# Optimization experiments

Measured on AMD Instinct MI355X. Metric: run time of the kernel, lower is better.

The kernel has to match this reference:

```python
import jax, jax.numpy as jnp
import numpy as np

SIZE = 8
STRIDES = (4, 8, 16)
QSCALE = 0.25
QMIN, QMAX = -32768, 32767  # qint16


def fake_quant(x):
    # QuantStub with FixedScaleObserver scale=0.25, qint16
    return jnp.clip(jnp.round(x / QSCALE), QMIN, QMAX) * QSCALE


def roi_align(f, rois, size):
    """torchvision.ops.RoIAlign(output_size=size, spatial_scale=1, sampling_ratio=1, aligned=False).
    f: [N,C,H,W], rois: [A,5] = (batch_idx, x1, y1, x2, y2) -> [A,C,size,size]."""
    N, C, H, W = f.shape
    b = rois[:, 0].astype(jnp.int32)
    x1, y1, x2, y2 = rois[:, 1], rois[:, 2], rois[:, 3], rois[:, 4]
    roi_w = jnp.maximum(x2 - x1, 1.0)
    roi_h = jnp.maximum(y2 - y1, 1.0)
    centers = jnp.arange(size, dtype=f.dtype) + 0.5  # sampling_ratio=1 -> bin center
    y = y1[:, None] + centers[None, :] * (roi_h / size)[:, None]  # [A,S]
    x = x1[:, None] + centers[None, :] * (roi_w / size)[:, None]  # [A,S]

    def prep(c, L):
        valid = (c >= -1.0) & (c <= L)
        c = jnp.maximum(c, 0.0)
        low0 = jnp.floor(c).astype(jnp.int32)
        hi_edge = low0 >= L - 1
        low = jnp.where(hi_edge, L - 1, low0)
        high = jnp.where(hi_edge, L - 1, low0 + 1)
        c = jnp.where(hi_edge, jnp.asarray(L - 1, c.dtype), c)
        frac = c - low.astype(c.dtype)
        return low, high, frac, valid

    yl, yh, fy, vy = prep(y, H)
    xl, xh, fx, vx = prep(x, W)

    ff = f.transpose(0, 2, 3, 1).reshape(N * H * W, C)  # channels-last flat for gather

    def gather(yy, xx):
        idx = (b[:, None, None] * H + yy[:, :, None]) * W + xx[:, None, :]  # [A,S,S]
        return ff[idx]  # [A,S,S,C]

    wy0 = (1.0 - fy)[:, :, None, None]
    wy1 = fy[:, :, None, None]
    wx0 = (1.0 - fx)[:, None, :, None]
    wx1 = fx[:, None, :, None]
    val = (gather(yl, xl) * wy0 * wx0 + gather(yl, xh) * wy0 * wx1
           + gather(yh, xl) * wy1 * wx0 + gather(yh, xh) * wy1 * wx1)
    mask = (vy[:, :, None] & vx[:, None, :])[..., None]
    val = jnp.where(mask, val, 0.0)
    return val.transpose(0, 3, 1, 2)  # [A,C,S,S]


def generate_rois(pixel, batch_index, size):
    bi = batch_index.astype(pixel.dtype)[:, None]
    rois = []
    for s in STRIDES:
        tl = jnp.maximum(pixel / s - size / 2.0, 0.0)
        br = jnp.maximum(pixel / s + size / 2.0, 0.0)
        rois.append(fake_quant(jnp.concatenate([bi, tl, br], axis=-1)))
    return rois


def setup_inputs() -> dict:
    key = jax.random.key(0)
    k0, k1, k2, kp, kb = jax.random.split(key, 5)
    f0 = jax.random.normal(k0, (4, 64, 256, 256), jnp.float32)
    f1 = jax.random.normal(k1, (4, 64, 128, 128), jnp.float32)
    f2 = jax.random.normal(k2, (4, 64, 64, 64), jnp.float32)
    pixel = jax.random.uniform(kp, (4096, 2), jnp.float32) * 1008.0  # raster-map coords
    batch_index = jax.random.randint(kb, (4096,), 0, 4, jnp.int32)
    return {"f0": f0, "f1": f1, "f2": f2, "pixel": pixel, "batch_index": batch_index}


def reference(f0, f1, f2, pixel, batch_index):
    rois = generate_rois(pixel, batch_index, SIZE)
    feats = [roi_align(f, r, SIZE) for f, r in zip((f0, f1, f2), rois)]
    return jnp.concatenate(feats, axis=1)  # [A, sum(C_i), SIZE, SIZE]
```

## Files before the change

### kernel.cpp

```cpp
#include <hip/hip_runtime.h>


#define NCH 64

typedef unsigned int  u32;
typedef unsigned short u16;

__device__ __forceinline__ float fake_quant(float v) {
    float r = rintf(v * 4.0f);
    r = fminf(fmaxf(r, -32768.0f), 32767.0f);
    return r * 0.25f;
}

struct Prep { int lo, hi; float fr; bool valid; };
__device__ __forceinline__ Prep prep(float c, int L) {
    Prep r;
    r.valid = (c >= -1.0f) && (c <= (float)L);
    c = fmaxf(c, 0.0f);
    const int l0 = (int)floorf(c);
    const bool he = (l0 >= L - 1);
    r.lo = he ? (L - 1) : l0;
    r.hi = he ? (L - 1) : (l0 + 1);
    r.fr = (he ? (float)(L - 1) : c) - (float)r.lo;
    return r;
}

__device__ __forceinline__ u16 f2bf(float x) {
    u32 u = __float_as_uint(x);
    u += 0x7FFFu + ((u >> 16) & 1u);
    return (u16)(u >> 16);
}
__device__ __forceinline__ float bflo(u32 w) { return __uint_as_float(w << 16); }
__device__ __forceinline__ float bfhi(u32 w) { return __uint_as_float(w & 0xFFFF0000u); }

__global__ __launch_bounds__(256) void nchw_to_nhwc_bf16(
    const float* __restrict__ f0, const float* __restrict__ f1,
    const float* __restrict__ f2, u16* __restrict__ n0,
    u16* __restrict__ n1, u16* __restrict__ n2)
{
    __shared__ float tile[64][65];
    const int t = threadIdx.x;
    const int b = blockIdx.y;
    const int g = blockIdx.x;
    const float* src; u16* dst; int HW; int tl;
    if (g < 1024)      { src = f0; dst = n0; HW = 65536; tl = g; }
    else if (g < 1280) { src = f1; dst = n1; HW = 16384; tl = g - 1024; }
    else               { src = f2; dst = n2; HW = 4096;  tl = g - 1280; }
    const int hw0 = tl * 64;
    const float* __restrict__ s = src + (size_t)b * 64 * HW + hw0;
    u32* __restrict__ d = (u32*)(dst + ((size_t)b * HW + hw0) * 64);

    const int x  = t & 63;
    const int ph = t >> 6;
    #pragma unroll
    for (int k = 0; k < 16; ++k) {
        const int c = ph * 16 + k;
        tile[c][x] = __builtin_nontemporal_load(s + (size_t)c * HW + x);
    }
    __syncthreads();
    #pragma unroll
    for (int k = 0; k < 8; ++k) {
        const int idx = k * 256 + t;
        const int pos = idx >> 5;
        const int cp  = idx & 31;
        const u32 w = (u32)f2bf(tile[2 * cp][pos])
                    | ((u32)f2bf(tile[2 * cp + 1][pos]) << 16);
        __builtin_nontemporal_store(w, d + pos * 32 + cp);
    }
}

__global__ __launch_bounds__(256) void cropper_qat_bf16(
    const u16* __restrict__ g0, const u16* __restrict__ g1,
    const u16* __restrict__ g2, const float* __restrict__ pixel,
    const int* __restrict__ bidx, float* __restrict__ out)
{
    __shared__ uint4 tile[81 * 8];

    const int a   = blockIdx.x;
    const int lvl = blockIdx.y;

    const float inv_s = (lvl == 0) ? 0.25f : (lvl == 1) ? 0.125f : 0.0625f;
    const int   L     = (lvl == 0) ? 256   : (lvl == 1) ? 128    : 64;
    const u16* __restrict__ f = (lvl == 0) ? g0 : (lvl == 1) ? g1 : g2;

    const int   b  = bidx[a];
    const float px = pixel[2 * a];
    const float py = pixel[2 * a + 1];

    const float x1 = fake_quant(fmaxf(px * inv_s - 4.0f, 0.0f));
    const float y1 = fake_quant(fmaxf(py * inv_s - 4.0f, 0.0f));
    const float x2 = fake_quant(fmaxf(px * inv_s + 4.0f, 0.0f));
    const float y2 = fake_quant(fmaxf(py * inv_s + 4.0f, 0.0f));

    const float binw = fmaxf(x2 - x1, 1.0f) * 0.125f;
    const float binh = fmaxf(y2 - y1, 1.0f) * 0.125f;

    const int y_lo = prep(y1 + 0.5f * binh, L).lo;
    const int x_lo = prep(x1 + 0.5f * binw, L).lo;

    const int tid = threadIdx.x;

    {
        const u16* __restrict__ fbase =
            f + ((size_t)b * L * L + (size_t)y_lo * L + x_lo) * NCH;
        #pragma unroll
        for (int it = 0; it < 3; ++it) {
            const int g = tid + it * 256;
            if (g < 648) {
                const int ly  = g / 72;
                const int rem = g - ly * 72;
                const int pos = ly * 9 + (rem >> 3);
                const int c   = rem & 7;
                const uint4 v = *(const uint4*)(fbase + (size_t)ly * L * NCH + rem * 8);
                tile[pos * 8 + (c ^ (pos & 7))] = v;
            }
        }
    }
    __syncthreads();

    const int p  = tid & 63;
    const int i  = p >> 3;
    const int j  = p & 7;
    const int c0 = tid >> 6;

    const Prep py_ = prep(y1 + ((float)i + 0.5f) * binh, L);
    const Prep px_ = prep(x1 + ((float)j + 0.5f) * binw, L);
    const bool valid = py_.valid && px_.valid;

    const float wy0 = 1.0f - py_.fr, wy1 = py_.fr;
    const float wx0 = 1.0f - px_.fr, wx1 = px_.fr;
    const float w00 = wy0 * wx0, w01 = wy0 * wx1;
    const float w10 = wy1 * wx0, w11 = wy1 * wx1;

    const int r0 = (py_.lo - y_lo) * 9;
    const int r1 = (py_.hi - y_lo) * 9;
    const int pos00 = r0 + (px_.lo - x_lo);
    const int pos01 = r0 + (px_.hi - x_lo);
    const int pos10 = r1 + (px_.lo - x_lo);
    const int pos11 = r1 + (px_.hi - x_lo);

    float r[16];
    #pragma unroll
    for (int k = 0; k < 16; ++k) r[k] = 0.0f;

    #define CORNER(POS, W) {                                                  \
        const uint4 qa = tile[(POS) * 8 + ((2 * c0)     ^ ((POS) & 7))];      \
        const uint4 qb = tile[(POS) * 8 + ((2 * c0 + 1) ^ ((POS) & 7))];      \
        r[0]  += bflo(qa.x) * (W); r[1]  += bfhi(qa.x) * (W);                 \
        r[2]  += bflo(qa.y) * (W); r[3]  += bfhi(qa.y) * (W);                 \
        r[4]  += bflo(qa.z) * (W); r[5]  += bfhi(qa.z) * (W);                 \
        r[6]  += bflo(qa.w) * (W); r[7]  += bfhi(qa.w) * (W);                 \
        r[8]  += bflo(qb.x) * (W); r[9]  += bfhi(qb.x) * (W);                 \
        r[10] += bflo(qb.y) * (W); r[11] += bfhi(qb.y) * (W);                 \
        r[12] += bflo(qb.z) * (W); r[13] += bfhi(qb.z) * (W);                 \
        r[14] += bflo(qb.w) * (W); r[15] += bfhi(qb.w) * (W); }

    CORNER(pos00, w00)
    CORNER(pos01, w01)
    CORNER(pos10, w10)
    CORNER(pos11, w11)
    #undef CORNER

    float* __restrict__ outp =
        out + ((size_t)a * 192 + (size_t)lvl * NCH + (size_t)c0 * 16) * 64 + p;
    #pragma unroll
    for (int k = 0; k < 16; ++k)
        __builtin_nontemporal_store(valid ? r[k] : 0.0f, outp + (size_t)k * 64);
}

__global__ __launch_bounds__(256) void cropper_qat_nchw(
    const float* __restrict__ f0, const float* __restrict__ f1,
    const float* __restrict__ f2, const float* __restrict__ pixel,
    const int* __restrict__ bidx, float* __restrict__ out)
{
    const int a   = blockIdx.x;
    const int lvl = blockIdx.y;
    const float inv_s = (lvl == 0) ? 0.25f : (lvl == 1) ? 0.125f : 0.0625f;
    const int   L     = (lvl == 0) ? 256   : (lvl == 1) ? 128    : 64;
    const float* __restrict__ f = (lvl == 0) ? f0 : (lvl == 1) ? f1 : f2;

    const int   b  = bidx[a];
    const float px = pixel[2 * a];
    const float py = pixel[2 * a + 1];
    const float x1 = fake_quant(fmaxf(px * inv_s - 4.0f, 0.0f));
    const float y1 = fake_quant(fmaxf(py * inv_s - 4.0f, 0.0f));
    const float x2 = fake_quant(fmaxf(px * inv_s + 4.0f, 0.0f));
    const float y2 = fake_quant(fmaxf(py * inv_s + 4.0f, 0.0f));
    const float binw = fmaxf(x2 - x1, 1.0f) * 0.125f;
    const float binh = fmaxf(y2 - y1, 1.0f) * 0.125f;

    const int tid = threadIdx.x;
    const int p = tid & 63, i = p >> 3, j = p & 7, c0 = tid >> 6;

    const Prep py_ = prep(y1 + ((float)i + 0.5f) * binh, L);
    const Prep px_ = prep(x1 + ((float)j + 0.5f) * binw, L);
    const bool valid = py_.valid && px_.valid;
    const float wy0 = 1.0f - py_.fr, wy1 = py_.fr;
    const float wx0 = 1.0f - px_.fr, wx1 = px_.fr;
    const float w00 = wy0 * wx0, w01 = wy0 * wx1, w10 = wy1 * wx0, w11 = wy1 * wx1;

    const size_t HW = (size_t)L * L;
    const float* __restrict__ fb = f + (size_t)b * NCH * HW;
    const int o00 = py_.lo * L + px_.lo, o01 = py_.lo * L + px_.hi;
    const int o10 = py_.hi * L + px_.lo, o11 = py_.hi * L + px_.hi;
    float* __restrict__ outp = out + ((size_t)a * 192 + (size_t)lvl * NCH) * 64 + p;

    #pragma unroll 4
    for (int c = c0; c < NCH; c += 4) {
        const float* __restrict__ fc = fb + (size_t)c * HW;
        float val = ((fc[o00] * w00 + fc[o01] * w01) + fc[o10] * w10) + fc[o11] * w11;
        outp[(size_t)c * 64] = valid ? val : 0.0f;
    }
}

extern "C" void kernel_launch(void* const* d_in, const int* in_sizes, int n_in,
                              void* d_out, int out_size, void* d_ws, size_t ws_size,
                              hipStream_t stream) {
    const float* f0    = (const float*)d_in[0];
    const float* f1    = (const float*)d_in[1];
    const float* f2    = (const float*)d_in[2];
    const float* pixel = (const float*)d_in[3];
    const int*   bidx  = (const int*)d_in[4];
    float* out = (float*)d_out;
    const int A = in_sizes[4];

    const size_t NEED = (size_t)(16777216 + 4194304 + 1048576) * 2 + 65536 + 4096;
    if (ws_size >= NEED) {
        u16* n0 = (u16*)d_ws;
        u16* n1 = n0 + 16777216;
        u16* n2 = n1 + 4194304;
        nchw_to_nhwc_bf16<<<dim3(1344, 4), 256, 0, stream>>>(f0, f1, f2, n0, n1, n2);
        cropper_qat_bf16<<<dim3(A, 3), 256, 0, stream>>>(n0, n1, n2, pixel, bidx, out);
    } else {
        cropper_qat_nchw<<<dim3(A, 3), 256, 0, stream>>>(f0, f1, f2, pixel, bidx, out);
    }
}
```

Before: 75.82 us.

## Vectorize transpose loads/stores and fuse three pyramid levels into one crop block

```diff
diff --git a/kernel.cpp b/kernel.cpp
--- a/kernel.cpp
+++ b/kernel.cpp
@@ -3,8 +3,10 @@
 
 #define NCH 64
 
-typedef unsigned int  u32;
+typedef unsigned int   u32;
 typedef unsigned short u16;
+typedef float  vf4 __attribute__((ext_vector_type(4)));
+typedef u32    vu2 __attribute__((ext_vector_type(2)));
 
 __device__ __forceinline__ float fake_quant(float v) {
     float r = rintf(v * 4.0f);
@@ -48,124 +50,141 @@
     else               { src = f2; dst = n2; HW = 4096;  tl = g - 1280; }
     const int hw0 = tl * 64;
     const float* __restrict__ s = src + (size_t)b * 64 * HW + hw0;
-    u32* __restrict__ d = (u32*)(dst + ((size_t)b * HW + hw0) * 64);
-
-    const int x  = t & 63;
-    const int ph = t >> 6;
-    #pragma unroll
-    for (int k = 0; k < 16; ++k) {
-        const int c = ph * 16 + k;
-        tile[c][x] = __builtin_nontemporal_load(s + (size_t)c * HW + x);
+    vu2* __restrict__ d = (vu2*)(dst + ((size_t)b * HW + hw0) * 64);
+
+    const int xq = (t & 15) * 4;
+    const int cb = t >> 4;
+    #pragma unroll
+    for (int k = 0; k < 4; ++k) {
+        const int c = k * 16 + cb;
+        const vf4 v = __builtin_nontemporal_load(
+            (const vf4*)(s + (size_t)c * HW + xq));
+        tile[c][xq + 0] = v.x;
+        tile[c][xq + 1] = v.y;
+        tile[c][xq + 2] = v.z;
+        tile[c][xq + 3] = v.w;
     }
     __syncthreads();
-    #pragma unroll
-    for (int k = 0; k < 8; ++k) {
+
+    #pragma unroll
+    for (int k = 0; k < 4; ++k) {
         const int idx = k * 256 + t;
-        const int pos = idx >> 5;
-        const int cp  = idx & 31;
-        const u32 w = (u32)f2bf(tile[2 * cp][pos])
-                    | ((u32)f2bf(tile[2 * cp + 1][pos]) << 16);
-        __builtin_nontemporal_store(w, d + pos * 32 + cp);
-    }
-}
-
-__global__ __launch_bounds__(256) void cropper_qat_bf16(
+        const int pos = idx >> 4;
+        const int c2  = idx & 15;
+        vu2 w;
+        w.x = (u32)f2bf(tile[4 * c2 + 0][pos])
+            | ((u32)f2bf(tile[4 * c2 + 1][pos]) << 16);
+        w.y = (u32)f2bf(tile[4 * c2 + 2][pos])
+            | ((u32)f2bf(tile[4 * c2 + 3][pos]) << 16);
+        __builtin_nontemporal_store(w, d + pos * 16 + c2);
+    }
+}
+
+__global__ __launch_bounds__(256) void cropper_qat_fused(
     const u16* __restrict__ g0, const u16* __restrict__ g1,
     const u16* __restrict__ g2, const float* __restrict__ pixel,
     const int* __restrict__ bidx, float* __restrict__ out)
 {
-    __shared__ uint4 tile[81 * 8];
+    __shared__ uint4 tile[3 * 648];
 
     const int a   = blockIdx.x;
-    const int lvl = blockIdx.y;
-
-    const float inv_s = (lvl == 0) ? 0.25f : (lvl == 1) ? 0.125f : 0.0625f;
-    const int   L     = (lvl == 0) ? 256   : (lvl == 1) ? 128    : 64;
-    const u16* __restrict__ f = (lvl == 0) ? g0 : (lvl == 1) ? g1 : g2;
-
-    const int   b  = bidx[a];
+    const int b   = bidx[a];
     const float px = pixel[2 * a];
     const float py = pixel[2 * a + 1];
-
-    const float x1 = fake_quant(fmaxf(px * inv_s - 4.0f, 0.0f));
-    const float y1 = fake_quant(fmaxf(py * inv_s - 4.0f, 0.0f));
-    const float x2 = fake_quant(fmaxf(px * inv_s + 4.0f, 0.0f));
-    const float y2 = fake_quant(fmaxf(py * inv_s + 4.0f, 0.0f));
-
-    const float binw = fmaxf(x2 - x1, 1.0f) * 0.125f;
-    const float binh = fmaxf(y2 - y1, 1.0f) * 0.125f;
-
-    const int y_lo = prep(y1 + 0.5f * binh, L).lo;
-    const int x_lo = prep(x1 + 0.5f * binw, L).lo;
-
     const int tid = threadIdx.x;
 
-    {
+    const int p  = tid & 63;
+    const int i  = p >> 3;
+    const int j  = p & 7;
+    const int c0 = tid >> 6;
+
+    float x1a[3], y1a[3], bwa[3], bha[3];
+    int   xla[3], yla[3];
+
+    #pragma unroll
+    for (int l = 0; l < 3; ++l) {
+        const float inv_s = (l == 0) ? 0.25f : (l == 1) ? 0.125f : 0.0625f;
+        const int   L     = (l == 0) ? 256   : (l == 1) ? 128    : 64;
+        const u16* __restrict__ f = (l == 0) ? g0 : (l == 1) ? g1 : g2;
+
+        const float x1 = fake_quant(fmaxf(px * inv_s - 4.0f, 0.0f));
+        const float y1 = fake_quant(fmaxf(py * inv_s - 4.0f, 0.0f));
+        const float x2 = fake_quant(fmaxf(px * inv_s + 4.0f, 0.0f));
+        const float y2 = fake_quant(fmaxf(py * inv_s + 4.0f, 0.0f));
+        const float bw = fmaxf(x2 - x1, 1.0f) * 0.125f;
+        const float bh = fmaxf(y2 - y1, 1.0f) * 0.125f;
+        const int y_lo = prep(y1 + 0.5f * bh, L).lo;
+        const int x_lo = prep(x1 + 0.5f * bw, L).lo;
+
+        x1a[l] = x1; y1a[l] = y1; bwa[l] = bw; bha[l] = bh;
+        xla[l] = x_lo; yla[l] = y_lo;
+
         const u16* __restrict__ fbase =
             f + ((size_t)b * L * L + (size_t)y_lo * L + x_lo) * NCH;
         #pragma unroll
         for (int it = 0; it < 3; ++it) {
-            const int g = tid + it * 256;
-            if (g < 648) {
-                const int ly  = g / 72;
-                const int rem = g - ly * 72;
+            const int gg = tid + it * 256;
+            if (gg < 648) {
+                const int ly  = gg / 72;
+                const int rem = gg - ly * 72;
                 const int pos = ly * 9 + (rem >> 3);
                 const int c   = rem & 7;
                 const uint4 v = *(const uint4*)(fbase + (size_t)ly * L * NCH + rem * 8);
-                tile[pos * 8 + (c ^ (pos & 7))] = v;
+                tile[l * 648 + pos * 8 + (c ^ (pos & 7))] = v;
             }
         }
     }
     __syncthreads();
 
-    const int p  = tid & 63;
-    const int i  = p >> 3;
-    const int j  = p & 7;
-    const int c0 = tid >> 6;
-
-    const Prep py_ = prep(y1 + ((float)i + 0.5f) * binh, L);
-    const Prep px_ = prep(x1 + ((float)j + 0.5f) * binw, L);
-    const bool valid = py_.valid && px_.valid;
-
-    const float wy0 = 1.0f - py_.fr, wy1 = py_.fr;
-    const float wx0 = 1.0f - px_.fr, wx1 = px_.fr;
-    const float w00 = wy0 * wx0, w01 = wy0 * wx1;
-    const float w10 = wy1 * wx0, w11 = wy1 * wx1;
-
-    const int r0 = (py_.lo - y_lo) * 9;
-    const int r1 = (py_.hi - y_lo) * 9;
-    const int pos00 = r0 + (px_.lo - x_lo);
-    const int pos01 = r0 + (px_.hi - x_lo);
-    const int pos10 = r1 + (px_.lo - x_lo);
-    const int pos11 = r1 + (px_.hi - x_lo);
-
-    float r[16];
-    #pragma unroll
-    for (int k = 0; k < 16; ++k) r[k] = 0.0f;
-
-    #define CORNER(POS, W) {                                                  \
-        const uint4 qa = tile[(POS) * 8 + ((2 * c0)     ^ ((POS) & 7))];      \
-        const uint4 qb = tile[(POS) * 8 + ((2 * c0 + 1) ^ ((POS) & 7))];      \
-        r[0]  += bflo(qa.x) * (W); r[1]  += bfhi(qa.x) * (W);                 \
-        r[2]  += bflo(qa.y) * (W); r[3]  += bfhi(qa.y) * (W);                 \
-        r[4]  += bflo(qa.z) * (W); r[5]  += bfhi(qa.z) * (W);                 \
-        r[6]  += bflo(qa.w) * (W); r[7]  += bfhi(qa.w) * (W);                 \
-        r[8]  += bflo(qb.x) * (W); r[9]  += bfhi(qb.x) * (W);                 \
-        r[10] += bflo(qb.y) * (W); r[11] += bfhi(qb.y) * (W);                 \
-        r[12] += bflo(qb.z) * (W); r[13] += bfhi(qb.z) * (W);                 \
-        r[14] += bflo(qb.w) * (W); r[15] += bfhi(qb.w) * (W); }
-
-    CORNER(pos00, w00)
-    CORNER(pos01, w01)
-    CORNER(pos10, w10)
-    CORNER(pos11, w11)
-    #undef CORNER
-
-    float* __restrict__ outp =
-        out + ((size_t)a * 192 + (size_t)lvl * NCH + (size_t)c0 * 16) * 64 + p;
-    #pragma unroll
-    for (int k = 0; k < 16; ++k)
-        __builtin_nontemporal_store(valid ? r[k] : 0.0f, outp + (size_t)k * 64);
+    #pragma unroll
+    for (int l = 0; l < 3; ++l) {
+        const int L = (l == 0) ? 256 : (l == 1) ? 128 : 64;
+        const uint4* __restrict__ tl = tile + l * 648;
+
+        const Prep py_ = prep(y1a[l] + ((float)i + 0.5f) * bha[l], L);
+        const Prep px_ = prep(x1a[l] + ((float)j + 0.5f) * bwa[l], L);
+        const bool valid = py_.valid && px_.valid;
+
+        const float wy0 = 1.0f - py_.fr, wy1 = py_.fr;
+        const float wx0 = 1.0f - px_.fr, wx1 = px_.fr;
+        const float w00 = wy0 * wx0, w01 = wy0 * wx1;
+        const float w10 = wy1 * wx0, w11 = wy1 * wx1;
+
+        const int r0 = (py_.lo - yla[l]) * 9;
+        const int r1 = (py_.hi - yla[l]) * 9;
+        const int pos00 = r0 + (px_.lo - xla[l]);
+        const int pos01 = r0 + (px_.hi - xla[l]);
+        const int pos10 = r1 + (px_.lo - xla[l]);
+        const int pos11 = r1 + (px_.hi - xla[l]);
+
+        float r[16];
+        #pragma unroll
+        for (int k = 0; k < 16; ++k) r[k] = 0.0f;
+
+        #define CORNER(POS, W) {                                              \
+            const uint4 qa = tl[(POS) * 8 + ((2 * c0)     ^ ((POS) & 7))];    \
+            const uint4 qb = tl[(POS) * 8 + ((2 * c0 + 1) ^ ((POS) & 7))];    \
+            r[0]  += bflo(qa.x) * (W); r[1]  += bfhi(qa.x) * (W);             \
+            r[2]  += bflo(qa.y) * (W); r[3]  += bfhi(qa.y) * (W);             \
+            r[4]  += bflo(qa.z) * (W); r[5]  += bfhi(qa.z) * (W);             \
+            r[6]  += bflo(qa.w) * (W); r[7]  += bfhi(qa.w) * (W);             \
+            r[8]  += bflo(qb.x) * (W); r[9]  += bfhi(qb.x) * (W);             \
+            r[10] += bflo(qb.y) * (W); r[11] += bfhi(qb.y) * (W);             \
+            r[12] += bflo(qb.z) * (W); r[13] += bfhi(qb.z) * (W);             \
+            r[14] += bflo(qb.w) * (W); r[15] += bfhi(qb.w) * (W); }
+
+        CORNER(pos00, w00)
+        CORNER(pos01, w01)
+        CORNER(pos10, w10)
+        CORNER(pos11, w11)
+        #undef CORNER
+
+        float* __restrict__ outp =
+            out + ((size_t)a * 192 + (size_t)l * NCH + (size_t)c0 * 16) * 64 + p;
+        #pragma unroll
+        for (int k = 0; k < 16; ++k)
+            __builtin_nontemporal_store(valid ? r[k] : 0.0f, outp + (size_t)k * 64);
+    }
 }
 
 __global__ __launch_bounds__(256) void cropper_qat_nchw(
@@ -224,13 +243,13 @@
     float* out = (float*)d_out;
     const int A = in_sizes[4];
 
-    const size_t NEED = (size_t)(16777216 + 4194304 + 1048576) * 2 + 65536 + 4096;
+    const size_t NEED = (size_t)(16777216 + 4194304 + 1048576) * 2 + 131072;
     if (ws_size >= NEED) {
         u16* n0 = (u16*)d_ws;
         u16* n1 = n0 + 16777216;
         u16* n2 = n1 + 4194304;
         nchw_to_nhwc_bf16<<<dim3(1344, 4), 256, 0, stream>>>(f0, f1, f2, n0, n1, n2);
-        cropper_qat_bf16<<<dim3(A, 3), 256, 0, stream>>>(n0, n1, n2, pixel, bidx, out);
+        cropper_qat_fused<<<dim3(A), 256, 0, stream>>>(n0, n1, n2, pixel, bidx, out);
     } else {
         cropper_qat_nchw<<<dim3(A, 3), 256, 0, stream>>>(f0, f1, f2, pixel, bidx, out);
     }
```

After: 83.22 us. +9.8%, slower.

## Fuse NCHW-to-NHWC bf16 conversion into cropper tile load, drop transpose pass

Applied to the files above, without the earlier changes.

```diff
diff --git a/kernel.cpp b/kernel.cpp
--- a/kernel.cpp
+++ b/kernel.cpp
@@ -3,7 +3,7 @@
 
 #define NCH 64
 
-typedef unsigned int  u32;
+typedef unsigned int   u32;
 typedef unsigned short u16;
 
 __device__ __forceinline__ float fake_quant(float v) {
@@ -33,45 +33,9 @@
 __device__ __forceinline__ float bflo(u32 w) { return __uint_as_float(w << 16); }
 __device__ __forceinline__ float bfhi(u32 w) { return __uint_as_float(w & 0xFFFF0000u); }
 
-__global__ __launch_bounds__(256) void nchw_to_nhwc_bf16(
+__global__ __launch_bounds__(256) void cropper_qat_fused(
     const float* __restrict__ f0, const float* __restrict__ f1,
-    const float* __restrict__ f2, u16* __restrict__ n0,
-    u16* __restrict__ n1, u16* __restrict__ n2)
-{
-    __shared__ float tile[64][65];
-    const int t = threadIdx.x;
-    const int b = blockIdx.y;
-    const int g = blockIdx.x;
-    const float* src; u16* dst; int HW; int tl;
-    if (g < 1024)      { src = f0; dst = n0; HW = 65536; tl = g; }
-    else if (g < 1280) { src = f1; dst = n1; HW = 16384; tl = g - 1024; }
-    else               { src = f2; dst = n2; HW = 4096;  tl = g - 1280; }
-    const int hw0 = tl * 64;
-    const float* __restrict__ s = src + (size_t)b * 64 * HW + hw0;
-    u32* __restrict__ d = (u32*)(dst + ((size_t)b * HW + hw0) * 64);
-
-    const int x  = t & 63;
-    const int ph = t >> 6;
-    #pragma unroll
-    for (int k = 0; k < 16; ++k) {
-        const int c = ph * 16 + k;
-        tile[c][x] = __builtin_nontemporal_load(s + (size_t)c * HW + x);
-    }
-    __syncthreads();
-    #pragma unroll
-    for (int k = 0; k < 8; ++k) {
-        const int idx = k * 256 + t;
-        const int pos = idx >> 5;
-        const int cp  = idx & 31;
-        const u32 w = (u32)f2bf(tile[2 * cp][pos])
-                    | ((u32)f2bf(tile[2 * cp + 1][pos]) << 16);
-        __builtin_nontemporal_store(w, d + pos * 32 + cp);
-    }
-}
-
-__global__ __launch_bounds__(256) void cropper_qat_bf16(
-    const u16* __restrict__ g0, const u16* __restrict__ g1,
-    const u16* __restrict__ g2, const float* __restrict__ pixel,
+    const float* __restrict__ f2, const float* __restrict__ pixel,
     const int* __restrict__ bidx, float* __restrict__ out)
 {
     __shared__ uint4 tile[81 * 8];
@@ -81,7 +45,7 @@
 
     const float inv_s = (lvl == 0) ? 0.25f : (lvl == 1) ? 0.125f : 0.0625f;
     const int   L     = (lvl == 0) ? 256   : (lvl == 1) ? 128    : 64;
-    const u16* __restrict__ f = (lvl == 0) ? g0 : (lvl == 1) ? g1 : g2;
+    const float* __restrict__ f = (lvl == 0) ? f0 : (lvl == 1) ? f1 : f2;
 
     const int   b  = bidx[a];
     const float px = pixel[2 * a];
@@ -101,18 +65,43 @@
     const int tid = threadIdx.x;
 
     {
-        const u16* __restrict__ fbase =
-            f + ((size_t)b * L * L + (size_t)y_lo * L + x_lo) * NCH;
+        const int xs    = x_lo & ~3;
+        const int off   = x_lo - xs;
+        const bool fastx = (xs + 12 <= L);
+        const float* __restrict__ fb = f + (size_t)b * NCH * L * L;
+        u16* __restrict__ tl16 = (u16*)tile;
+
         #pragma unroll
         for (int it = 0; it < 3; ++it) {
-            const int g = tid + it * 256;
-            if (g < 648) {
-                const int ly  = g / 72;
-                const int rem = g - ly * 72;
-                const int pos = ly * 9 + (rem >> 3);
-                const int c   = rem & 7;
-                const uint4 v = *(const uint4*)(fbase + (size_t)ly * L * NCH + rem * 8);
-                tile[pos * 8 + (c ^ (pos & 7))] = v;
+            const int u = tid + it * 256;
+            if (u < 576) {
+                const int row = u >> 6;
+                const int c   = u & 63;
+                const int row_g = (y_lo + row <= L - 1) ? (y_lo + row) : (L - 1);
+                const float* __restrict__ rp =
+                    fb + (size_t)c * L * L + (size_t)row_g * L;
+                float v[12];
+                if (fastx) {
+                    const float4 a0 = *(const float4*)(rp + xs);
+                    const float4 a1 = *(const float4*)(rp + xs + 4);
+                    const float4 a2 = *(const float4*)(rp + xs + 8);
+                    v[0] = a0.x; v[1] = a0.y; v[2]  = a0.z; v[3]  = a0.w;
+                    v[4] = a1.x; v[5] = a1.y; v[6]  = a1.z; v[7]  = a1.w;
+                    v[8] = a2.x; v[9] = a2.y; v[10] = a2.z; v[11] = a2.w;
+                } else {
+                    #pragma unroll
+                    for (int k = 0; k < 12; ++k) {
+                        const int xg = (xs + k <= L - 1) ? (xs + k) : (L - 1);
+                        v[k] = rp[xg];
+                    }
+                }
+                const int cq = c >> 3;
+                const int ce = c & 7;
+                #pragma unroll
+                for (int k = 0; k < 9; ++k) {
+                    const int pos = row * 9 + k;
+                    tl16[pos * 64 + (cq ^ (pos & 7)) * 8 + ce] = f2bf(v[off + k]);
+                }
             }
         }
     }
@@ -168,51 +157,6 @@
         __builtin_nontemporal_store(valid ? r[k] : 0.0f, outp + (size_t)k * 64);
 }
 
-__global__ __launch_bounds__(256) void cropper_qat_nchw(
-    const float* __restrict__ f0, const float* __restrict__ f1,
-    const float* __restrict__ f2, const float* __restrict__ pixel,
-    const int* __restrict__ bidx, float* __restrict__ out)
-{
-    const int a   = blockIdx.x;
-    const int lvl = blockIdx.y;
-    const float inv_s = (lvl == 0) ? 0.25f : (lvl == 1) ? 0.125f : 0.0625f;
-    const int   L     = (lvl == 0) ? 256   : (lvl == 1) ? 128    : 64;
-    const float* __restrict__ f = (lvl == 0) ? f0 : (lvl == 1) ? f1 : f2;
-
-    const int   b  = bidx[a];
-    const float px = pixel[2 * a];
-    const float py = pixel[2 * a + 1];
-    const float x1 = fake_quant(fmaxf(px * inv_s - 4.0f, 0.0f));
-    const float y1 = fake_quant(fmaxf(py * inv_s - 4.0f, 0.0f));
-    const float x2 = fake_quant(fmaxf(px * inv_s + 4.0f, 0.0f));
-    const float y2 = fake_quant(fmaxf(py * inv_s + 4.0f, 0.0f));
-    const float binw = fmaxf(x2 - x1, 1.0f) * 0.125f;
-    const float binh = fmaxf(y2 - y1, 1.0f) * 0.125f;
-
-    const int tid = threadIdx.x;
-    const int p = tid & 63, i = p >> 3, j = p & 7, c0 = tid >> 6;
-
-    const Prep py_ = prep(y1 + ((float)i + 0.5f) * binh, L);
-    const Prep px_ = prep(x1 + ((float)j + 0.5f) * binw, L);
-    const bool valid = py_.valid && px_.valid;
-    const float wy0 = 1.0f - py_.fr, wy1 = py_.fr;
-    const float wx0 = 1.0f - px_.fr, wx1 = px_.fr;
-    const float w00 = wy0 * wx0, w01 = wy0 * wx1, w10 = wy1 * wx0, w11 = wy1 * wx1;
-
-    const size_t HW = (size_t)L * L;
-    const float* __restrict__ fb = f + (size_t)b * NCH * HW;
-    const int o00 = py_.lo * L + px_.lo, o01 = py_.lo * L + px_.hi;
-    const int o10 = py_.hi * L + px_.lo, o11 = py_.hi * L + px_.hi;
-    float* __restrict__ outp = out + ((size_t)a * 192 + (size_t)lvl * NCH) * 64 + p;
-
-    #pragma unroll 4
-    for (int c = c0; c < NCH; c += 4) {
-        const float* __restrict__ fc = fb + (size_t)c * HW;
-        float val = ((fc[o00] * w00 + fc[o01] * w01) + fc[o10] * w10) + fc[o11] * w11;
-        outp[(size_t)c * 64] = valid ? val : 0.0f;
-    }
-}
-
 extern "C" void kernel_launch(void* const* d_in, const int* in_sizes, int n_in,
                               void* d_out, int out_size, void* d_ws, size_t ws_size,
                               hipStream_t stream) {
@@ -224,14 +168,5 @@
     float* out = (float*)d_out;
     const int A = in_sizes[4];
 
-    const size_t NEED = (size_t)(16777216 + 4194304 + 1048576) * 2 + 65536 + 4096;
-    if (ws_size >= NEED) {
-        u16* n0 = (u16*)d_ws;
-        u16* n1 = n0 + 16777216;
-        u16* n2 = n1 + 4194304;
-        nchw_to_nhwc_bf16<<<dim3(1344, 4), 256, 0, stream>>>(f0, f1, f2, n0, n1, n2);
-        cropper_qat_bf16<<<dim3(A, 3), 256, 0, stream>>>(n0, n1, n2, pixel, bidx, out);
-    } else {
-        cropper_qat_nchw<<<dim3(A, 3), 256, 0, stream>>>(f0, f1, f2, pixel, bidx, out);
-    }
+    cropper_qat_fused<<<dim3(A, 3), 256, 0, stream>>>(f0, f1, f2, pixel, bidx, out);
 }
```

Result: slower. 135.3 us (+78.5%).
